# Kernel optimization log

Hardware: AMD Instinct MI355X
Metric: run time of the kernel (lower is better)

The kernel has to match this reference:

```python
import jax, jax.numpy as jnp
import numpy as np
import math

B, S, DIM = 1, 2048, 4096
N_HEADS, N_KV, HEAD_DIM = 32, 8, 128
WINDOW = 2048
ROPE_THETA = 10000.0


def setup_inputs() -> dict:
    key = jax.random.key(0)
    ks = jax.random.split(key, 6)
    w_std = 0.02
    x = jax.random.normal(ks[0], (B, S, DIM), dtype=jnp.float32)
    wq = jax.random.normal(ks[1], (DIM, N_HEADS * HEAD_DIM), dtype=jnp.float32) * w_std
    wk = jax.random.normal(ks[2], (DIM, N_KV * HEAD_DIM), dtype=jnp.float32) * w_std
    wv = jax.random.normal(ks[3], (DIM, N_KV * HEAD_DIM), dtype=jnp.float32) * w_std
    wo = jax.random.normal(ks[4], (N_HEADS * HEAD_DIM, DIM), dtype=jnp.float32) * w_std
    # rotary tables (real/imag of complex_rotary_matrix)
    pos = jnp.arange(S, dtype=jnp.float32)
    inv_freq = 1.0 / (ROPE_THETA ** (jnp.arange(0, HEAD_DIM, 2, dtype=jnp.float32) / HEAD_DIM))
    angles = pos[:, None] * inv_freq[None, :]  # [S, HEAD_DIM/2]
    cos, sin = jnp.cos(angles), jnp.sin(angles)
    positions = jnp.arange(S, dtype=jnp.int32)
    # sliding-window causal additive mask: allow j <= i and i - j < WINDOW
    i = jnp.arange(S)[:, None]
    j = jnp.arange(S)[None, :]
    allowed = (j <= i) & (i - j < WINDOW)
    mask = jnp.where(allowed, 0.0, -jnp.inf).astype(jnp.float32)
    cache_k = jnp.zeros((B, WINDOW, N_KV, HEAD_DIM), dtype=jnp.float32)
    cache_v = jnp.zeros((B, WINDOW, N_KV, HEAD_DIM), dtype=jnp.float32)
    return dict(x=x, wq=wq, wk=wk, wv=wv, wo=wo, cos=cos, sin=sin,
                positions=positions, mask=mask, cache_k=cache_k, cache_v=cache_v)


def _apply_rope(t, cos, sin):
    # t: [B, S, H, D]; interleaved complex pairs as in torch.view_as_complex
    tp = t.reshape(*t.shape[:-1], HEAD_DIM // 2, 2)
    te, to = tp[..., 0], tp[..., 1]
    c = cos[None, :, None, :]
    s = sin[None, :, None, :]
    re = te * c - to * s
    im = te * s + to * c
    return jnp.stack([re, im], axis=-1).reshape(t.shape)


def reference(x, wq, wk, wv, wo, cos, sin, positions, mask, cache_k, cache_v):
    repeats = N_HEADS // N_KV
    q = (x @ wq).reshape(B, S, N_HEADS, HEAD_DIM)
    k = (x @ wk).reshape(B, S, N_KV, HEAD_DIM)
    v = (x @ wv).reshape(B, S, N_KV, HEAD_DIM)
    q = _apply_rope(q, cos, sin)
    k = _apply_rope(k, cos, sin)
    # rolling KV-cache scatter update (prefill path: positions.shape[0] > 1)
    scatter_pos = positions[-WINDOW:] % WINDOW
    new_cache_k = cache_k.at[:, scatter_pos].set(k[:, -WINDOW:])
    new_cache_v = cache_v.at[:, scatter_pos].set(v[:, -WINDOW:])
    # GQA head repetition (repeat_kv_head)
    k = jnp.repeat(k, repeats, axis=2)  # [B, S, N_HEADS, D]
    v = jnp.repeat(v, repeats, axis=2)
    scores = jnp.einsum('bqhd,bkhd->bhqk', q, k) / math.sqrt(HEAD_DIM)
    scores = scores + mask[None, None, :, :]
    attn = jax.nn.softmax(scores.astype(jnp.float32), axis=-1).astype(q.dtype)
    out = jnp.einsum('bhqk,bkhd->bqhd', attn, v)
    out = out.reshape(B, S, N_HEADS * HEAD_DIM)
    return out @ wo, new_cache_k, new_cache_v
```

## Files before the change

kernel.cpp:

```cpp
#include <hip/hip_runtime.h>

typedef __bf16 bf16;
typedef __bf16 bf16x8 __attribute__((ext_vector_type(8)));
typedef __bf16 bf16x4 __attribute__((ext_vector_type(4)));
typedef float  f32x4  __attribute__((ext_vector_type(4)));

__device__ __forceinline__ f32x4 mfma16(bf16x8 a, bf16x8 b, f32x4 c) {
  return __builtin_amdgcn_mfma_f32_16x16x32_bf16(a, b, c, 0, 0, 0);
}

__device__ __forceinline__ void gload16(const bf16* g, bf16* l) {
  __builtin_amdgcn_global_load_lds(
      (const __attribute__((address_space(1))) void*)g,
      (__attribute__((address_space(3))) void*)l, 16, 0, 0);
}

__global__ void cast_x_kernel(const float* __restrict__ in, bf16* __restrict__ out) {
  const int i = blockIdx.x * 256 + threadIdx.x;
  const float4 v = ((const float4*)in)[i];
  bf16x4 o;
  o[0] = (bf16)v.x; o[1] = (bf16)v.y; o[2] = (bf16)v.z; o[3] = (bf16)v.w;
  *(bf16x4*)&out[(size_t)i * 4] = o;
}

__global__ void transpose_cast(const float* __restrict__ in, bf16* __restrict__ out,
                               int ldin, int ldout) {
  __shared__ bf16 t[32][33];
  const int c0 = blockIdx.x * 32, r0 = blockIdx.y * 32;
  const int x = threadIdx.x, y = threadIdx.y;
  #pragma unroll
  for (int i = 0; i < 32; i += 8)
    t[y + i][x] = (bf16)in[(size_t)(r0 + y + i) * ldin + c0 + x];
  __syncthreads();
  #pragma unroll
  for (int i = 0; i < 32; i += 8)
    out[(size_t)(c0 + y + i) * ldout + r0 + x] = t[x][y + i];
}

__global__ void permute_v(const bf16* __restrict__ qkv, bf16* __restrict__ vp) {
  __shared__ bf16 t[32][33];
  const int sb  = blockIdx.x;
  const int kvh = blockIdx.y >> 2;
  const int dt  = blockIdx.y & 3;
  const int x = threadIdx.x, y = threadIdx.y;
  #pragma unroll
  for (int i = 0; i < 32; i += 8)
    t[y + i][x] = qkv[(size_t)(sb * 32 + y + i) * 6144 + 5120 + kvh * 128 + dt * 32 + x];
  __syncthreads();
  #pragma unroll
  for (int i = 0; i < 32; i += 8)
    vp[((size_t)(kvh * 64 + sb) * 128 + dt * 32 + y + i) * 32 + x] = t[x][y + i];
}

template <typename OutT>
__global__ __launch_bounds__(256, 2)
void gemm_bt(const bf16* __restrict__ A, const bf16* __restrict__ Bt,
             OutT* __restrict__ C, int M, int N, int K, int ldc) {
  __shared__ __attribute__((aligned(16))) bf16 As[128 * 64];
  __shared__ __attribute__((aligned(16))) bf16 Bs[128 * 64];
  const int tid  = threadIdx.x;
  const int wave = tid >> 6;
  const int lane = tid & 63;
  const int l15  = lane & 15;
  const int lg   = lane >> 4;
  const int bm = blockIdx.y * 128;
  const int bn = blockIdx.x * 128;
  const int wr = (wave >> 1) * 64;
  const int wc = (wave & 1) * 64;

  const int srow = wave * 32 + (lane >> 3);
  const int scol = (lane & 7) * 8;
  const bf16* agp = A  + (size_t)(bm + srow) * K + scol;
  const bf16* bgp = Bt + (size_t)(bn + srow) * K + scol;
  bf16* al = &As[wave * 2048];
  bf16* bl = &Bs[wave * 2048];

  f32x4 acc[4][4] = {};

  for (int k0 = 0; k0 < K; k0 += 64) {
    __syncthreads();
    #pragma unroll
    for (int rnd = 0; rnd < 4; ++rnd)
      gload16(agp + (size_t)rnd * 8 * K + k0, al + rnd * 512);
    #pragma unroll
    for (int rnd = 0; rnd < 4; ++rnd)
      gload16(bgp + (size_t)rnd * 8 * K + k0, bl + rnd * 512);
    __syncthreads();
    #pragma unroll
    for (int kk = 0; kk < 64; kk += 32) {
      bf16x8 bq[4];
      #pragma unroll
      for (int ni = 0; ni < 4; ++ni)
        bq[ni] = *(const bf16x8*)&Bs[(wc + ni * 16 + l15) * 64 + kk + lg * 8];
      #pragma unroll
      for (int mi = 0; mi < 4; ++mi) {
        bf16x8 aq = *(const bf16x8*)&As[(wr + mi * 16 + l15) * 64 + kk + lg * 8];
        #pragma unroll
        for (int ni = 0; ni < 4; ++ni)
          acc[mi][ni] = mfma16(aq, bq[ni], acc[mi][ni]);
      }
    }
  }
  #pragma unroll
  for (int mi = 0; mi < 4; ++mi)
    #pragma unroll
    for (int ni = 0; ni < 4; ++ni)
      #pragma unroll
      for (int r = 0; r < 4; ++r)
        C[(size_t)(bm + wr + mi * 16 + lg * 4 + r) * ldc + (bn + wc + ni * 16 + l15)] =
            (OutT)acc[mi][ni][r];
}

__global__ void rope_q_kernel(bf16* __restrict__ q, const float* __restrict__ cs,
                              const float* __restrict__ sn) {
  const int idx = blockIdx.x * 256 + threadIdx.x;
  const int p  = idx & 63;
  const int sh = idx >> 6;
  const int h  = sh & 31;
  const int s  = sh >> 5;
  const float c  = cs[s * 64 + p];
  const float si = sn[s * 64 + p];
  const size_t ii = (size_t)s * 6144 + h * 128 + 2 * p;
  const float te = (float)q[ii], to = (float)q[ii + 1];
  q[ii]     = (bf16)(te * c - to * si);
  q[ii + 1] = (bf16)(te * si + to * c);
}

__global__ void rope_k_kernel(const bf16* __restrict__ qkv, bf16* __restrict__ kp,
                              float* __restrict__ ck, const float* __restrict__ cs,
                              const float* __restrict__ sn) {
  const int idx = blockIdx.x * 256 + threadIdx.x;
  const int p  = idx & 63;
  const int sh = idx >> 6;
  const int h  = sh & 7;
  const int s  = sh >> 3;
  const float c  = cs[s * 64 + p];
  const float si = sn[s * 64 + p];
  const size_t ii = (size_t)s * 6144 + 4096 + h * 128 + 2 * p;
  const float te = (float)qkv[ii], to = (float)qkv[ii + 1];
  const float re = te * c - to * si;
  const float im = te * si + to * c;
  const size_t io = ((size_t)(h * 4 + (p >> 4)) * 2048 + s) * 32 + ((2 * p) & 31);
  kp[io]     = (bf16)re;
  kp[io + 1] = (bf16)im;
  const size_t ic = (size_t)s * 1024 + h * 128 + 2 * p;
  ck[ic]     = re;
  ck[ic + 1] = im;
}

__global__ void cast_v_kernel(const bf16* __restrict__ qkv, float* __restrict__ cv) {
  const int i = blockIdx.x * 256 + threadIdx.x;
  const int s = i >> 8;
  const int c = (i & 255) * 4;
  const bf16x4 v = *(const bf16x4*)&qkv[(size_t)s * 6144 + 5120 + c];
  float4 o;
  o.x = (float)v[0]; o.y = (float)v[1]; o.z = (float)v[2]; o.w = (float)v[3];
  *(float4*)&cv[(size_t)s * 1024 + c] = o;
}

__global__ __launch_bounds__(256, 3)
void attn_fwd(const bf16* __restrict__ Q, const bf16* __restrict__ Kp,
              const bf16* __restrict__ Vp, bf16* __restrict__ O) {
  __shared__ __attribute__((aligned(16))) bf16 Kb[8192];
  __shared__ __attribute__((aligned(16))) bf16 Vb[8192];
  __shared__ __attribute__((aligned(16))) bf16 P_lds[4][16][72];
  const int id   = blockIdx.x;
  const int qt   = 31 - (id >> 5);
  const int kvh  = id & 7;
  const int sub  = (id >> 3) & 3;
  const int h    = kvh * 4 + sub;
  const int t    = threadIdx.x;
  const int w    = t >> 6;
  const int lane = t & 63;
  const int l15  = lane & 15;
  const int lg   = lane >> 4;
  const float scale = 0.08838834764831845f;
  const bf16* Kh = Kp + (size_t)kvh * 262144;
  const bf16* Vh = Vp + (size_t)kvh * 262144;
  const int koff = (t >> 2) * 32 + (t & 3) * 8;

  const int qw  = qt * 64 + w * 16;
  const int myq = qw + l15;

  bf16x8 qf[4];
  #pragma unroll
  for (int ds = 0; ds < 4; ++ds)
    qf[ds] = *(const bf16x8*)&Q[(size_t)myq * 6144 + h * 128 + ds * 32 + lg * 8];

  f32x4 o[8] = {};
  float m = -1e30f, ell = 0.f;

  #pragma unroll
  for (int i = 0; i < 4; ++i)
    gload16(Kh + (size_t)i * 65536 + koff, Kb + i * 2048 + w * 512);
  #pragma unroll
  for (int i = 0; i < 4; ++i)
    gload16(Vh + (size_t)i * 2048 + koff, Vb + i * 2048 + w * 512);
  __syncthreads();

  #pragma unroll 1
  for (int kt = 0; kt <= qt; ++kt) {
    f32x4 T[4] = {};
    __builtin_amdgcn_s_setprio(1);
    #pragma unroll
    for (int kb = 0; kb < 4; ++kb)
      #pragma unroll
      for (int ds = 0; ds < 4; ++ds) {
        bf16x8 kf = *(const bf16x8*)&Kb[(ds * 64 + kb * 16 + l15) * 32 + lg * 8];
        T[kb] = mfma16(kf, qf[ds], T[kb]);
      }
    __builtin_amdgcn_s_setprio(0);
    __syncthreads();
    if (kt < qt) {
      #pragma unroll
      for (int i = 0; i < 4; ++i)
        gload16(Kh + (size_t)i * 65536 + (kt + 1) * 2048 + koff,
                Kb + i * 2048 + w * 512);
    }

    float pv[16];
    float pmax = -1e30f;
    if (kt == qt) {
      #pragma unroll
      for (int kb = 0; kb < 4; ++kb)
        #pragma unroll
        for (int r = 0; r < 4; ++r) {
          const int key = qt * 64 + kb * 16 + lg * 4 + r;
          const float s = (key > myq) ? -1e30f : T[kb][r] * scale;
          pv[kb * 4 + r] = s;
          pmax = fmaxf(pmax, s);
        }
    } else {
      #pragma unroll
      for (int kb = 0; kb < 4; ++kb)
        #pragma unroll
        for (int r = 0; r < 4; ++r) {
          const float s = T[kb][r] * scale;
          pv[kb * 4 + r] = s;
          pmax = fmaxf(pmax, s);
        }
    }
    float base = m;
    if (!__all(pmax - m <= 8.f)) {
      float wmax = pmax;
      wmax = fmaxf(wmax, __shfl_xor(wmax, 16));
      wmax = fmaxf(wmax, __shfl_xor(wmax, 32));
      const float newm = fmaxf(m, wmax);
      const float corr = __expf(m - newm);
      ell *= corr;
      m = newm; base = newm;
      float sf[4];
      #pragma unroll
      for (int r = 0; r < 4; ++r) sf[r] = __shfl(corr, lg * 4 + r);
      #pragma unroll
      for (int df = 0; df < 8; ++df)
        #pragma unroll
        for (int r = 0; r < 4; ++r) o[df][r] *= sf[r];
    }
    bf16 pb[16];
    float tsum = 0.f;
    #pragma unroll
    for (int i = 0; i < 16; ++i) {
      const float p = __expf(pv[i] - base);
      tsum += p;
      pb[i] = (bf16)p;
    }
    ell += tsum;

    #pragma unroll
    for (int kb = 0; kb < 4; ++kb) {
      bf16x4 pk;
      pk[0] = pb[kb * 4 + 0]; pk[1] = pb[kb * 4 + 1];
      pk[2] = pb[kb * 4 + 2]; pk[3] = pb[kb * 4 + 3];
      *(bf16x4*)&P_lds[w][l15][kb * 16 + lg * 4] = pk;
    }
    __builtin_amdgcn_s_setprio(1);
    #pragma unroll
    for (int ks = 0; ks < 2; ++ks) {
      bf16x8 pa = *(const bf16x8*)&P_lds[w][l15][ks * 32 + lg * 8];
      #pragma unroll
      for (int df = 0; df < 8; ++df) {
        bf16x8 vf = *(const bf16x8*)&Vb[(ks * 128 + df * 16 + l15) * 32 + lg * 8];
        o[df] = mfma16(pa, vf, o[df]);
      }
    }
    __builtin_amdgcn_s_setprio(0);
    __syncthreads();
    if (kt < qt) {
      #pragma unroll
      for (int i = 0; i < 4; ++i)
        gload16(Vh + (size_t)(kt + 1) * 8192 + i * 2048 + koff,
                Vb + i * 2048 + w * 512);
    }
  }

  ell += __shfl_xor(ell, 16);
  ell += __shfl_xor(ell, 32);
  float er[4];
  #pragma unroll
  for (int r = 0; r < 4; ++r) er[r] = 1.f / __shfl(ell, lg * 4 + r);
  #pragma unroll
  for (int df = 0; df < 8; ++df)
    #pragma unroll
    for (int r = 0; r < 4; ++r)
      O[(size_t)(qw + lg * 4 + r) * 4096 + h * 128 + df * 16 + l15] =
          (bf16)(o[df][r] * er[r]);
}

extern "C" void kernel_launch(void* const* d_in, const int* in_sizes, int n_in,
                              void* d_out, int out_size, void* d_ws, size_t ws_size,
                              hipStream_t stream) {
  const float* x    = (const float*)d_in[0];
  const float* wq   = (const float*)d_in[1];
  const float* wk   = (const float*)d_in[2];
  const float* wv   = (const float*)d_in[3];
  const float* wo   = (const float*)d_in[4];
  const float* cosf_ = (const float*)d_in[5];
  const float* sinf_ = (const float*)d_in[6];

  float* out     = (float*)d_out;
  float* cache_k = out + (size_t)8388608;
  float* cache_v = cache_k + (size_t)2097152;
  bf16* qkv = (bf16*)d_out;

  bf16* ws = (bf16*)d_ws;
  bf16* wT = ws;
  bf16* kp = ws + (size_t)25165824;
  bf16* vp = kp + (size_t)2097152;
  bf16* xb = vp + (size_t)2097152;
  bf16* aout = xb;

  const dim3 tb(32, 8);
  cast_x_kernel<<<8192, 256, 0, stream>>>(x, xb);
  transpose_cast<<<dim3(128, 128), tb, 0, stream>>>(wq, wT, 4096, 4096);
  transpose_cast<<<dim3(32, 128), tb, 0, stream>>>(wk, wT + (size_t)16777216,
                                                   1024, 4096);
  transpose_cast<<<dim3(32, 128), tb, 0, stream>>>(wv, wT + (size_t)20971520,
                                                   1024, 4096);
  gemm_bt<bf16><<<dim3(48, 16), 256, 0, stream>>>(xb, wT, qkv, 2048, 6144, 4096, 6144);
  rope_q_kernel<<<16384, 256, 0, stream>>>(qkv, cosf_, sinf_);
  rope_k_kernel<<<4096, 256, 0, stream>>>(qkv, kp, cache_k, cosf_, sinf_);
  cast_v_kernel<<<2048, 256, 0, stream>>>(qkv, cache_v);
  permute_v<<<dim3(64, 32), tb, 0, stream>>>(qkv, vp);
  transpose_cast<<<dim3(128, 128), tb, 0, stream>>>(wo, wT, 4096, 4096);
  attn_fwd<<<1024, 256, 0, stream>>>(qkv, kp, vp, aout);
  gemm_bt<float><<<dim3(32, 16), 256, 0, stream>>>(aout, wT, out, 2048, 4096, 4096, 4096);
}
```

Baseline: 360.3 us.

## Replace GEMM with 256x256-tile, 8-wave double-buffered, swizzled LDS pipeline

Replaces the simple 128x128 single-buffered bf16 GEMM with a 512-thread kernel that computes 256x256 output tiles. Global-to-LDS loads for the next K tile are issued while MFMAs run on the current one, using two LDS buffers, s_setprio phases and explicit waitcnt/barrier control. LDS addresses are XOR-swizzled to avoid bank conflicts. The larger tiles give more data reuse, but they leave only 192 and 128 blocks, which underfills a 256-CU device, and they use 128KB of LDS per block.

```diff
diff --git a/kernel.cpp b/kernel.cpp
--- a/kernel.cpp
+++ b/kernel.cpp
@@ -52,63 +52,148 @@
     vp[((size_t)(kvh * 64 + sb) * 128 + dt * 32 + y + i) * 32 + x] = t[x][y + i];
 }
 
+#define MMQ(MB, NB)                                                            \
+  _Pragma("unroll")                                                            \
+  for (int mi = 0; mi < 4; ++mi)                                               \
+    _Pragma("unroll")                                                          \
+    for (int ni = 0; ni < 2; ++ni)                                             \
+      _Pragma("unroll")                                                        \
+      for (int kk = 0; kk < 2; ++kk)                                           \
+        acc[MB + mi][NB + ni] =                                                \
+            mfma16(ar[mi][kk], br[NB + ni][kk], acc[MB + mi][NB + ni]);
+
+#define PH_OPEN                                                                \
+  __builtin_amdgcn_s_barrier();                                                \
+  asm volatile("s_waitcnt lgkmcnt(0)" ::: "memory");                           \
+  __builtin_amdgcn_s_setprio(1);
+
+#define PH_CLOSE                                                               \
+  __builtin_amdgcn_s_setprio(0);                                               \
+  __builtin_amdgcn_s_barrier();
+
 template <typename OutT>
-__global__ __launch_bounds__(256, 2)
-void gemm_bt(const bf16* __restrict__ A, const bf16* __restrict__ Bt,
-             OutT* __restrict__ C, int M, int N, int K, int ldc) {
-  __shared__ __attribute__((aligned(16))) bf16 As[128 * 64];
-  __shared__ __attribute__((aligned(16))) bf16 Bs[128 * 64];
-  const int tid  = threadIdx.x;
-  const int wave = tid >> 6;
-  const int lane = tid & 63;
+__global__ __launch_bounds__(512, 2)
+void gemm8(const bf16* __restrict__ A, const bf16* __restrict__ Bt,
+           OutT* __restrict__ C, int M, int N, int K, int ldc) {
+  __shared__ __attribute__((aligned(16))) bf16 lds[65536];
+  char* ldsc = (char*)lds;
+  constexpr int AO0 = 0, BO0 = 32768, AO1 = 65536, BO1 = 98304;
+
+  const int t    = threadIdx.x;
+  const int w    = t >> 6;
+  const int lane = t & 63;
   const int l15  = lane & 15;
   const int lg   = lane >> 4;
-  const int bm = blockIdx.y * 128;
-  const int bn = blockIdx.x * 128;
-  const int wr = (wave >> 1) * 64;
-  const int wc = (wave & 1) * 64;
-
-  const int srow = wave * 32 + (lane >> 3);
-  const int scol = (lane & 7) * 8;
-  const bf16* agp = A  + (size_t)(bm + srow) * K + scol;
-  const bf16* bgp = Bt + (size_t)(bn + srow) * K + scol;
-  bf16* al = &As[wave * 2048];
-  bf16* bl = &Bs[wave * 2048];
-
-  f32x4 acc[4][4] = {};
-
-  for (int k0 = 0; k0 < K; k0 += 64) {
-    __syncthreads();
-    #pragma unroll
-    for (int rnd = 0; rnd < 4; ++rnd)
-      gload16(agp + (size_t)rnd * 8 * K + k0, al + rnd * 512);
-    #pragma unroll
-    for (int rnd = 0; rnd < 4; ++rnd)
-      gload16(bgp + (size_t)rnd * 8 * K + k0, bl + rnd * 512);
-    __syncthreads();
-    #pragma unroll
-    for (int kk = 0; kk < 64; kk += 32) {
-      bf16x8 bq[4];
-      #pragma unroll
-      for (int ni = 0; ni < 4; ++ni)
-        bq[ni] = *(const bf16x8*)&Bs[(wc + ni * 16 + l15) * 64 + kk + lg * 8];
-      #pragma unroll
-      for (int mi = 0; mi < 4; ++mi) {
-        bf16x8 aq = *(const bf16x8*)&As[(wr + mi * 16 + l15) * 64 + kk + lg * 8];
-        #pragma unroll
-        for (int ni = 0; ni < 4; ++ni)
-          acc[mi][ni] = mfma16(aq, bq[ni], acc[mi][ni]);
-      }
-    }
+  const int wm   = w >> 2;
+  const int wn   = w & 3;
+  const int hb   = wn >> 1;
+  const int bm   = (blockIdx.x & 7) * 256;
+  const int bn   = (blockIdx.x >> 3) * 256;
+
+  const int d0     = t * 16;
+  const int dsw    = d0 ^ (((d0 >> 9) & 1) << 5);
+  const int srow_s = (dsw >> 6) & 127;
+  const int scol_e = (dsw & 63) >> 1;
+
+  auto stg = [&](const bf16* P, int rowbase, int tile, int half, int region) {
+    const bf16* s = P + (size_t)(rowbase + half * 128 + srow_s) * K + tile * 64 + scol_e;
+    gload16(s,      (bf16*)(ldsc + region + half * 16384 + w * 1024));
+    gload16(s + 32, (bf16*)(ldsc + region + half * 16384 + 8192 + w * 1024));
+  };
+  auto lda = [&](int AO, int m, int kk) -> bf16x8 {
+    int byte = AO + wm * 16384 + kk * 8192 + (m * 16 + l15) * 64 + lg * 16;
+    byte ^= ((byte >> 9) & 1) << 5;
+    return *(const bf16x8*)(ldsc + byte);
+  };
+  auto ldb = [&](int BO, int n, int kk) -> bf16x8 {
+    int byte = BO + hb * 16384 + kk * 8192 +
+               ((wn & 1) * 64 + n * 16 + l15) * 64 + lg * 16;
+    byte ^= ((byte >> 9) & 1) << 5;
+    return *(const bf16x8*)(ldsc + byte);
+  };
+
+  f32x4 acc[8][4] = {};
+  bf16x8 ar[4][2], br[4][2];
+
+  const int NT = K >> 6;
+  const int NI = K >> 7;
+
+  stg(A,  bm, 0, 0, AO0);  stg(A,  bm, 0, 1, AO0);
+  stg(Bt, bn, 0, 0, BO0);  stg(Bt, bn, 0, 1, BO0);
+  stg(Bt, bn, 1, 0, BO1);  stg(Bt, bn, 1, 1, BO1);
+  asm volatile("s_waitcnt vmcnt(4)" ::: "memory");
+  __builtin_amdgcn_s_barrier();
+
+  #pragma unroll 1
+  for (int it = 0; it < NI; ++it) {
+    const int t1 = 2 * it + 1;
+    const int t2 = (2 * it + 2 < NT) ? 2 * it + 2 : NT - 1;
+    const int t3 = (2 * it + 3 < NT) ? 2 * it + 3 : NT - 1;
+
+    #pragma unroll
+    for (int mi = 0; mi < 4; ++mi) {
+      ar[mi][0] = lda(AO0, mi, 0); ar[mi][1] = lda(AO0, mi, 1);
+    }
+    #pragma unroll
+    for (int ni = 0; ni < 2; ++ni) {
+      br[ni][0] = ldb(BO0, ni, 0); br[ni][1] = ldb(BO0, ni, 1);
+    }
+    stg(A, bm, t1, 0, AO1);
+    PH_OPEN; MMQ(0, 0); PH_CLOSE;
+    #pragma unroll
+    for (int ni = 2; ni < 4; ++ni) {
+      br[ni][0] = ldb(BO0, ni, 0); br[ni][1] = ldb(BO0, ni, 1);
+    }
+    stg(A, bm, t1, 1, AO1);
+    PH_OPEN; MMQ(0, 2); PH_CLOSE;
+    #pragma unroll
+    for (int mi = 0; mi < 4; ++mi) {
+      ar[mi][0] = lda(AO0, 4 + mi, 0); ar[mi][1] = lda(AO0, 4 + mi, 1);
+    }
+    stg(Bt, bn, t2, 0, BO0);
+    PH_OPEN; MMQ(4, 0); PH_CLOSE;
+    stg(Bt, bn, t2, 1, BO0);
+    PH_OPEN; MMQ(4, 2);
+    __builtin_amdgcn_s_setprio(0);
+    asm volatile("s_waitcnt vmcnt(4)" ::: "memory");
+    __builtin_amdgcn_s_barrier();
+    #pragma unroll
+    for (int mi = 0; mi < 4; ++mi) {
+      ar[mi][0] = lda(AO1, mi, 0); ar[mi][1] = lda(AO1, mi, 1);
+    }
+    #pragma unroll
+    for (int ni = 0; ni < 2; ++ni) {
+      br[ni][0] = ldb(BO1, ni, 0); br[ni][1] = ldb(BO1, ni, 1);
+    }
+    stg(A, bm, t2, 0, AO0);
+    PH_OPEN; MMQ(0, 0); PH_CLOSE;
+    #pragma unroll
+    for (int ni = 2; ni < 4; ++ni) {
+      br[ni][0] = ldb(BO1, ni, 0); br[ni][1] = ldb(BO1, ni, 1);
+    }
+    stg(A, bm, t2, 1, AO0);
+    PH_OPEN; MMQ(0, 2); PH_CLOSE;
+    #pragma unroll
+    for (int mi = 0; mi < 4; ++mi) {
+      ar[mi][0] = lda(AO1, 4 + mi, 0); ar[mi][1] = lda(AO1, 4 + mi, 1);
+    }
+    stg(Bt, bn, t3, 0, BO1);
+    PH_OPEN; MMQ(4, 0); PH_CLOSE;
+    stg(Bt, bn, t3, 1, BO1);
+    PH_OPEN; MMQ(4, 2);
+    __builtin_amdgcn_s_setprio(0);
+    asm volatile("s_waitcnt vmcnt(4)" ::: "memory");
+    __builtin_amdgcn_s_barrier();
   }
-  #pragma unroll
-  for (int mi = 0; mi < 4; ++mi)
+
+  #pragma unroll
+  for (int mi = 0; mi < 8; ++mi)
     #pragma unroll
     for (int ni = 0; ni < 4; ++ni)
       #pragma unroll
-      for (int r = 0; r < 4; ++r)
-        C[(size_t)(bm + wr + mi * 16 + lg * 4 + r) * ldc + (bn + wc + ni * 16 + l15)] =
-            (OutT)acc[mi][ni][r];
+      for (int rr = 0; rr < 4; ++rr)
+        C[(size_t)(bm + wm * 128 + mi * 16 + lg * 4 + rr) * ldc +
+          (bn + wn * 64 + ni * 16 + l15)] = (OutT)acc[mi][ni][rr];
 }
 
 __global__ void rope_q_kernel(bf16* __restrict__ q, const float* __restrict__ cs,
@@ -337,12 +422,12 @@
                                                    1024, 4096);
   transpose_cast<<<dim3(32, 128), tb, 0, stream>>>(wv, wT + (size_t)20971520,
                                                    1024, 4096);
-  gemm_bt<bf16><<<dim3(48, 16), 256, 0, stream>>>(xb, wT, qkv, 2048, 6144, 4096, 6144);
+  gemm8<bf16><<<192, 512, 0, stream>>>(xb, wT, qkv, 2048, 6144, 4096, 6144);
   rope_q_kernel<<<16384, 256, 0, stream>>>(qkv, cosf_, sinf_);
   rope_k_kernel<<<4096, 256, 0, stream>>>(qkv, kp, cache_k, cosf_, sinf_);
   cast_v_kernel<<<2048, 256, 0, stream>>>(qkv, cache_v);
   permute_v<<<dim3(64, 32), tb, 0, stream>>>(qkv, vp);
   transpose_cast<<<dim3(128, 128), tb, 0, stream>>>(wo, wT, 4096, 4096);
   attn_fwd<<<1024, 256, 0, stream>>>(qkv, kp, vp, aout);
-  gemm_bt<float><<<dim3(32, 16), 256, 0, stream>>>(aout, wT, out, 2048, 4096, 4096, 4096);
-}
+  gemm8<float><<<128, 512, 0, stream>>>(aout, wT, out, 2048, 4096, 4096, 4096);
+}
```

Result: no change. 362.2 us (+0.5%).
